# Kernel optimization log

Hardware: AMD Instinct MI355X
Metric: run time of the kernel (lower is better)

The kernel has to match this reference:

```python
import jax, jax.numpy as jnp
import numpy as np

B, S, E = 4, 1024, 1024
H, DK, HS = 16, 64, 64
FF = 4096
EPS = 1e-6


def _layernorm(x, g, b):
    mu = jnp.mean(x, axis=-1, keepdims=True)
    var = jnp.mean((x - mu) ** 2, axis=-1, keepdims=True)
    return (x - mu) * jax.lax.rsqrt(var + EPS) * g + b


def setup_inputs() -> dict:
    key = jax.random.key(0)
    ks = jax.random.split(key, 20)
    s_e = 1.0 / np.sqrt(E)
    s_ff = 1.0 / np.sqrt(FF)
    d = {
        "x": jax.random.normal(ks[0], (B, S, E), jnp.float32),
        "pos_encoding": jax.random.normal(ks[1], (S, S, 8), jnp.float32),
        # weights stored [in, out] (torch Linear transposed)
        "Wq": jax.random.normal(ks[2], (E, H * DK), jnp.float32) * s_e,
        "bq": jnp.zeros((H * DK,), jnp.float32),
        "Wk": jax.random.normal(ks[3], (E, H * DK), jnp.float32) * s_e,
        "bk": jnp.zeros((H * DK,), jnp.float32),
        "Wv": jax.random.normal(ks[4], (E, H * HS), jnp.float32) * s_e,
        "bv": jnp.zeros((H * HS,), jnp.float32),
        "Wo": jax.random.normal(ks[5], (H * HS, E), jnp.float32) * s_e,
        "bo": jnp.zeros((E,), jnp.float32),
        "Wg": jax.random.normal(ks[6], (E, E), jnp.float32) * s_e,
        "bg": jnp.zeros((E,), jnp.float32),
        "Wf1": jax.random.normal(ks[7], (E, FF), jnp.float32) * s_e,
        "bf1": jnp.zeros((FF,), jnp.float32),
        "Wfg": jax.random.normal(ks[8], (E, FF), jnp.float32) * s_e,
        "bfg": jnp.zeros((FF,), jnp.float32),
        "Wf2": jax.random.normal(ks[9], (FF, E), jnp.float32) * s_ff,
        "bf2": jnp.zeros((E,), jnp.float32),
        "ln1_g": jnp.ones((E,), jnp.float32),
        "ln1_b": jnp.zeros((E,), jnp.float32),
        "ln2_g": jnp.ones((E,), jnp.float32),
        "ln2_b": jnp.zeros((E,), jnp.float32),
    }
    return d


def reference(x, pos_encoding, Wq, bq, Wk, bk, Wv, bv, Wo, bo, Wg, bg,
              Wf1, bf1, Wfg, bfg, Wf2, bf2, ln1_g, ln1_b, ln2_g, ln2_b):
    b, s, _ = x.shape
    q = (x @ Wq + bq).reshape(b, s, H, DK)
    k = (x @ Wk + bk).reshape(b, s, H, DK)
    v = (x @ Wv + bv).reshape(b, s, H, HS)
    scale = jnp.sqrt(jnp.float32(DK))
    # [b, h, q, k]
    scores = jnp.einsum("bqhd,bkhd->bhqk", q, k) / scale
    pos_bias = jnp.mean(pos_encoding[:s, :s, :], axis=-1)  # [s, s]
    scores = scores + pos_bias[None, None, :, :]
    probs = jax.nn.softmax(scores, axis=-1)
    ctx = jnp.einsum("bhqk,bkhd->bqhd", probs, v).reshape(b, s, H * HS)
    attn_out = ctx @ Wo + bo
    attn_out = jax.nn.sigmoid(x @ Wg + bg) * attn_out
    x1 = _layernorm(x + attn_out, ln1_g, ln1_b)
    ff = (x1 @ Wf1 + bf1) * jax.nn.sigmoid(x1 @ Wfg + bfg)
    ff = ff @ Wf2 + bf2
    return _layernorm(x1 + ff, ln2_g, ln2_b)
```

## Files before the change

kernel.cpp:

```cpp
#include <hip/hip_runtime.h>

constexpr int NB = 4, NS = 1024, NE = 1024, NH = 16, NFF = 4096;
constexpr int NM = NB * NS;

typedef short s8v __attribute__((ext_vector_type(8)));
typedef short s4v __attribute__((ext_vector_type(4)));
typedef float f4  __attribute__((ext_vector_type(4)));

__device__ __forceinline__ float b2f(unsigned short u) {
    union { unsigned int i; float f; } v; v.i = ((unsigned int)u) << 16; return v.f;
}
__device__ __forceinline__ unsigned short f2b(float f) {
    union { float f; unsigned int i; } v; v.f = f;
    unsigned int r = v.i + 0x7FFFu + ((v.i >> 16) & 1u);
    return (unsigned short)(r >> 16);
}
__device__ __forceinline__ float sigf(float x) { return 1.f / (1.f + __expf(-x)); }

#define GL2LDS(g, l) __builtin_amdgcn_global_load_lds( \
    (const __attribute__((address_space(1))) void*)(g), \
    (__attribute__((address_space(3))) void*)(l), 16, 0, 0)

__global__ __launch_bounds__(256) void cvt_x_kernel(
    const float* __restrict__ X, unsigned short* __restrict__ O)
{
    size_t i = ((size_t)blockIdx.x * 256 + threadIdx.x) * 8;
    f4 v0 = *(const f4*)(X + i), v1 = *(const f4*)(X + i + 4);
    s8v o;
#pragma unroll
    for (int j = 0; j < 4; j++) { o[j] = (short)f2b(v0[j]); o[4 + j] = (short)f2b(v1[j]); }
    *(s8v*)(O + i) = o;
}

__global__ __launch_bounds__(256) void cvt_t_kernel(
    const float* s0, const float* s1, const float* s2, const float* s3, const float* s4,
    unsigned short* d0, unsigned short* d1, unsigned short* d2, unsigned short* d3,
    unsigned short* d4, int K, int N)
{
    const int z = blockIdx.z;
    const float* W = (z == 0) ? s0 : (z == 1) ? s1 : (z == 2) ? s2 : (z == 3) ? s3 : s4;
    unsigned short* WT = (z == 0) ? d0 : (z == 1) ? d1 : (z == 2) ? d2 : (z == 3) ? d3 : d4;
    __shared__ unsigned short L[64][72];
    const int k0 = blockIdx.y * 64, n0 = blockIdx.x * 64;
    const int t = threadIdx.x;
    const int r = t >> 4, c4 = (t & 15) * 4;
#pragma unroll
    for (int p = 0; p < 4; p++) {
        int k = r + p * 16;
        f4 v = *(const f4*)&W[(size_t)(k0 + k) * N + n0 + c4];
#pragma unroll
        for (int i = 0; i < 4; i++) L[c4 + i][k] = f2b(v[i]);
    }
    __syncthreads();
    const int n = t >> 2, kc = (t & 3) * 16;
    s8v o0, o1;
#pragma unroll
    for (int i = 0; i < 8; i++) { o0[i] = (short)L[n][kc + i]; o1[i] = (short)L[n][kc + 8 + i]; }
    unsigned short* dst = WT + (size_t)(n0 + n) * K + k0 + kc;
    *(s8v*)dst = o0; *(s8v*)(dst + 8) = o1;
}

__global__ __launch_bounds__(256) void posmean_kernel(
    const float* __restrict__ pe, float* __restrict__ bias)
{
    int idx = blockIdx.x * 256 + threadIdx.x;
    const float* p = pe + (size_t)idx * 8;
    f4 v0 = *(const f4*)p, v1 = *(const f4*)(p + 4);
    float s = 0.f;
#pragma unroll
    for (int i = 0; i < 4; i++) s += v0[i] + v1[i];
    bias[idx] = (s * 0.125f - 8.0f) * 1.44269504f;
}

#define EPI_QKVG     0
#define EPI_GATE_RES 2
#define EPI_RES      4
#define EPI_BIAS     5

template <int EPI, int TM>
__global__ __launch_bounds__(256) void gemm_bt(
    const unsigned short* __restrict__ A,
    const unsigned short* __restrict__ BT,
    const float* b0p, const float* b1p, const float* b2p, const float* b3p,
    const unsigned short* ex1,
    const unsigned short* ex2,
    unsigned short* C, int M, int N, int K)
{
    constexpr int AR = 32 * TM;
    __shared__ short As0[AR * 32], As1[AR * 32];
    __shared__ short Bs0[128 * 32], Bs1[128 * 32];

    const int tid  = threadIdx.x;
    const int m0   = blockIdx.y * AR;
    const int n0   = blockIdx.x * 128;
    const int lane = tid & 63;
    const int wave = tid >> 6;
    const int wm   = (wave >> 1) * (16 * TM), wn = (wave & 1) * 64;
    const int quad = lane >> 4, lo = lane & 15;
    const int lrow = lane >> 2;
    const int lcol = (((lane & 3) ^ ((lane >> 4) & 3))) * 8;
    const int rcol = ((quad ^ ((lo >> 2) & 3))) * 8;

    f4 acc[TM][4];
#pragma unroll
    for (int i = 0; i < TM; i++)
#pragma unroll
        for (int j = 0; j < 4; j++)
#pragma unroll
            for (int r = 0; r < 4; r++) acc[i][j][r] = 0.f;

    const unsigned short* ga = A  + (size_t)(m0 + wave * (AR / 4) + lrow) * K + lcol;
    const unsigned short* gb = BT + (size_t)(n0 + wave * 32 + lrow) * K + lcol;
    short* lA0  = &As0[(wave * (AR / 4)) * 32];
    short* lA1  = &As1[(wave * (AR / 4)) * 32];
    short* lB00 = &Bs0[(wave * 32) * 32];
    short* lB01 = &Bs0[(wave * 32 + 16) * 32];
    short* lB10 = &Bs1[(wave * 32) * 32];
    short* lB11 = &Bs1[(wave * 32 + 16) * 32];

    for (int k0 = 0; k0 < K; k0 += 64) {
#pragma unroll
        for (int t = 0; t < TM / 2; t++) {
            GL2LDS(ga + k0 +      (size_t)t * 16 * K, lA0 + t * 16 * 32);
            GL2LDS(ga + k0 + 32 + (size_t)t * 16 * K, lA1 + t * 16 * 32);
        }
        GL2LDS(gb + k0,               lB00);
        GL2LDS(gb + k0 + 16 * K,      lB01);
        GL2LDS(gb + k0 + 32,          lB10);
        GL2LDS(gb + k0 + 32 + 16 * K, lB11);
        __syncthreads();

        s8v af[TM], bf[4];
#pragma unroll
        for (int i = 0; i < TM; i++)
            af[i] = *(const s8v*)&As0[(wm + i * 16 + lo) * 32 + rcol];
#pragma unroll
        for (int j = 0; j < 4; j++)
            bf[j] = *(const s8v*)&Bs0[(wn + j * 16 + lo) * 32 + rcol];
#pragma unroll
        for (int i = 0; i < TM; i++)
#pragma unroll
            for (int j = 0; j < 4; j++)
                acc[i][j] = __builtin_amdgcn_mfma_f32_16x16x32_bf16(af[i], bf[j], acc[i][j], 0, 0, 0);
#pragma unroll
        for (int i = 0; i < TM; i++)
            af[i] = *(const s8v*)&As1[(wm + i * 16 + lo) * 32 + rcol];
#pragma unroll
        for (int j = 0; j < 4; j++)
            bf[j] = *(const s8v*)&Bs1[(wn + j * 16 + lo) * 32 + rcol];
#pragma unroll
        for (int i = 0; i < TM; i++)
#pragma unroll
            for (int j = 0; j < 4; j++)
                acc[i][j] = __builtin_amdgcn_mfma_f32_16x16x32_bf16(af[i], bf[j], acc[i][j], 0, 0, 0);
        __syncthreads();
    }

    const float* bp = b0p;
    bool do_sig = false;
    if (EPI == EPI_QKVG) {
        int seg = n0 >> 10;
        bp = (seg == 0) ? b0p : (seg == 1) ? b1p : (seg == 2) ? b2p : b3p;
        do_sig = (n0 >= 3072);
    }

#pragma unroll
    for (int i = 0; i < TM; i++) {
#pragma unroll
        for (int j = 0; j < 4; j++) {
#pragma unroll
            for (int r = 0; r < 4; r++) {
                int gm = m0 + wm + i * 16 + quad * 4 + r;
                int gn = n0 + wn + j * 16 + lo;
                size_t idx = (size_t)gm * N + gn;
                float v = acc[i][j][r] + (EPI == EPI_QKVG ? bp[gn & 1023] : bp[gn]);
                if (EPI == EPI_QKVG)          { if (do_sig) v = sigf(v); }
                else if (EPI == EPI_GATE_RES) v = b2f(ex1[idx]) + b2f(ex2[(size_t)gm * 4096 + gn]) * v;
                else if (EPI == EPI_RES)      v = b2f(ex1[idx]) + v;
                C[idx] = f2b(v);
            }
        }
    }
}

template <int TM>
__global__ __launch_bounds__(256) void gemm_ff(
    const unsigned short* __restrict__ A,
    const unsigned short* __restrict__ B1T,
    const unsigned short* __restrict__ B2T,
    const float* __restrict__ bias1, const float* __restrict__ bias2,
    unsigned short* __restrict__ C, int M, int N, int K)
{
    constexpr int AR = 32 * TM;
    __shared__ short As[AR * 32];
    __shared__ short B1s[128 * 32];
    __shared__ short B2s[128 * 32];

    const int tid  = threadIdx.x;
    const int m0   = blockIdx.y * AR;
    const int n0   = blockIdx.x * 128;
    const int lane = tid & 63;
    const int wave = tid >> 6;
    const int wm   = (wave >> 1) * (16 * TM), wn = (wave & 1) * 64;
    const int quad = lane >> 4, lo = lane & 15;
    const int lrow = lane >> 2;
    const int lcol = (((lane & 3) ^ ((lane >> 4) & 3))) * 8;
    const int rcol = ((quad ^ ((lo >> 2) & 3))) * 8;

    f4 accA[TM][4], accB[TM][4];
#pragma unroll
    for (int i = 0; i < TM; i++)
#pragma unroll
        for (int j = 0; j < 4; j++)
#pragma unroll
            for (int r = 0; r < 4; r++) { accA[i][j][r] = 0.f; accB[i][j][r] = 0.f; }

    const unsigned short* ga  = A   + (size_t)(m0 + wave * (AR / 4) + lrow) * K + lcol;
    const unsigned short* gb1 = B1T + (size_t)(n0 + wave * 32 + lrow) * K + lcol;
    const unsigned short* gb2 = B2T + (size_t)(n0 + wave * 32 + lrow) * K + lcol;
    short* lA   = &As[(wave * (AR / 4)) * 32];
    short* lB10 = &B1s[(wave * 32) * 32];
    short* lB11 = &B1s[(wave * 32 + 16) * 32];
    short* lB20 = &B2s[(wave * 32) * 32];
    short* lB21 = &B2s[(wave * 32 + 16) * 32];

    for (int k0 = 0; k0 < K; k0 += 32) {
#pragma unroll
        for (int t = 0; t < TM / 2; t++)
            GL2LDS(ga + k0 + (size_t)t * 16 * K, lA + t * 16 * 32);
        GL2LDS(gb1 + k0,          lB10);
        GL2LDS(gb1 + k0 + 16 * K, lB11);
        GL2LDS(gb2 + k0,          lB20);
        GL2LDS(gb2 + k0 + 16 * K, lB21);
        __syncthreads();

        s8v af[TM], b1f[4], b2f_[4];
#pragma unroll
        for (int i = 0; i < TM; i++)
            af[i] = *(const s8v*)&As[(wm + i * 16 + lo) * 32 + rcol];
#pragma unroll
        for (int j = 0; j < 4; j++) {
            b1f[j]  = *(const s8v*)&B1s[(wn + j * 16 + lo) * 32 + rcol];
            b2f_[j] = *(const s8v*)&B2s[(wn + j * 16 + lo) * 32 + rcol];
        }
#pragma unroll
        for (int i = 0; i < TM; i++)
#pragma unroll
            for (int j = 0; j < 4; j++) {
                accA[i][j] = __builtin_amdgcn_mfma_f32_16x16x32_bf16(af[i], b1f[j],  accA[i][j], 0, 0, 0);
                accB[i][j] = __builtin_amdgcn_mfma_f32_16x16x32_bf16(af[i], b2f_[j], accB[i][j], 0, 0, 0);
            }
        __syncthreads();
    }

#pragma unroll
    for (int i = 0; i < TM; i++) {
#pragma unroll
        for (int j = 0; j < 4; j++) {
#pragma unroll
            for (int r = 0; r < 4; r++) {
                int gm = m0 + wm + i * 16 + quad * 4 + r;
                int gn = n0 + wn + j * 16 + lo;
                float a = accA[i][j][r] + bias1[gn];
                float g = accB[i][j][r] + bias2[gn];
                C[(size_t)gm * N + gn] = f2b(a * sigf(g));
            }
        }
    }
}

__global__ __launch_bounds__(256) void attn_kernel(
    const unsigned short* __restrict__ QKVG, const float* __restrict__ bias,
    unsigned short* __restrict__ ctx)
{
    __shared__ short Ks[32 * 72];
    __shared__ short Vt[64 * 48];
    __shared__ short Ps[4][16 * 40];

    const int tid = threadIdx.x;
    const int lane = tid & 63, wave = tid >> 6;
    const int quad = lane >> 4, lo = lane & 15;
    const int bh = blockIdx.y;
    const int b = bh >> 4, h = bh & 15;
    const int q0 = blockIdx.x * 64 + wave * 16;
    const size_t base  = (size_t)b * NS * 4096 + (size_t)h * 64;
    const size_t baseK = base + 1024, baseV = base + 2048;
    constexpr float c1 = 0.125f * 1.44269504f;

    s8v aq0 = *(const s8v*)(QKVG + base + (size_t)(q0 + lo) * 4096 + quad * 8);
    s8v aq1 = *(const s8v*)(QKVG + base + (size_t)(q0 + lo) * 4096 + 32 + quad * 8);

    f4 accO[4];
    float l_r[4];
#pragma unroll
    for (int r = 0; r < 4; r++) {
        l_r[r] = 0.f;
#pragma unroll
        for (int j = 0; j < 4; j++) accO[j][r] = 0.f;
    }

    const int skv = tid >> 3, sd8 = (tid & 7) * 8;
    const int vkv = tid & 31, vd8 = (tid >> 5) * 8;
    const int pvk = 2 * (vkv & 15) + (vkv >> 4);

    s8v kk = *(const s8v*)(QKVG + baseK + (size_t)skv * 4096 + sd8);
    s8v vv = *(const s8v*)(QKVG + baseV + (size_t)vkv * 4096 + vd8);

    for (int kv0 = 0; kv0 < NS; kv0 += 32) {
        *(s8v*)&Ks[skv * 72 + sd8] = kk;
#pragma unroll
        for (int i = 0; i < 8; i++) Vt[(vd8 + i) * 48 + pvk] = (short)vv[i];
        __syncthreads();

        s8v kkn = kk, vvn = vv;
        if (kv0 + 32 < NS) {
            kkn = *(const s8v*)(QKVG + baseK + (size_t)(kv0 + 32 + skv) * 4096 + sd8);
            vvn = *(const s8v*)(QKVG + baseV + (size_t)(kv0 + 32 + vkv) * 4096 + vd8);
        }

        f4 sc[2];
#pragma unroll
        for (int cb = 0; cb < 2; cb++) {
            s8v bk0 = *(const s8v*)&Ks[(cb * 16 + lo) * 72 + quad * 8];
            s8v bk1 = *(const s8v*)&Ks[(cb * 16 + lo) * 72 + 32 + quad * 8];
            f4 z;
#pragma unroll
            for (int r = 0; r < 4; r++) z[r] = 0.f;
            z = __builtin_amdgcn_mfma_f32_16x16x32_bf16(aq0, bk0, z, 0, 0, 0);
            sc[cb] = __builtin_amdgcn_mfma_f32_16x16x32_bf16(aq1, bk1, z, 0, 0, 0);
        }

        int* PsI = (int*)&Ps[wave][0];
#pragma unroll
        for (int r = 0; r < 4; r++) {
            int qrow = q0 + quad * 4 + r;
            const float* bp = &bias[(size_t)qrow * NS + kv0];
            float p0 = exp2f(sc[0][r] * c1 + bp[lo]);
            float p1 = exp2f(sc[1][r] * c1 + bp[16 + lo]);
            l_r[r] += p0 + p1;
            unsigned int pk = (unsigned int)f2b(p0) | ((unsigned int)f2b(p1) << 16);
            PsI[(quad * 4 + r) * 20 + lo] = (int)pk;
        }
        s8v pf = *(const s8v*)&Ps[wave][lo * 40 + quad * 8];
#pragma unroll
        for (int j = 0; j < 4; j++) {
            s8v bv = *(const s8v*)&Vt[(j * 16 + lo) * 48 + quad * 8];
            accO[j] = __builtin_amdgcn_mfma_f32_16x16x32_bf16(pf, bv, accO[j], 0, 0, 0);
        }
        __syncthreads();
        kk = kkn; vv = vvn;
    }

#pragma unroll
    for (int r = 0; r < 4; r++) {
        float l = l_r[r];
#pragma unroll
        for (int d = 1; d < 16; d <<= 1) l += __shfl_xor(l, d, 64);
        l_r[r] = 1.f / l;
    }
#pragma unroll
    for (int j = 0; j < 4; j++)
#pragma unroll
        for (int r = 0; r < 4; r++) {
            int qrow = q0 + quad * 4 + r;
            ctx[((size_t)b * NS + qrow) * 1024 + h * 64 + j * 16 + lo] = f2b(accO[j][r] * l_r[r]);
        }
}

__global__ __launch_bounds__(256) void ln_kernel(
    const unsigned short* __restrict__ X, const float* __restrict__ g,
    const float* __restrict__ bb, void* __restrict__ out, int outF32)
{
    const int row = blockIdx.x;
    const unsigned short* xr = X + (size_t)row * NE;
    s4v xv = *(const s4v*)(xr + threadIdx.x * 4);
    float v[4], s = 0.f, ss = 0.f;
#pragma unroll
    for (int i = 0; i < 4; i++) {
        v[i] = b2f((unsigned short)xv[i]);
        s += v[i]; ss += v[i] * v[i];
    }
#pragma unroll
    for (int d = 1; d < 64; d <<= 1) { s += __shfl_xor(s, d, 64); ss += __shfl_xor(ss, d, 64); }
    __shared__ float red[8];
    int wave = threadIdx.x >> 6, lane = threadIdx.x & 63;
    if (lane == 0) { red[wave] = s; red[4 + wave] = ss; }
    __syncthreads();
    s  = red[0] + red[1] + red[2] + red[3];
    ss = red[4] + red[5] + red[6] + red[7];
    float mu = s * (1.f / NE);
    float var = ss * (1.f / NE) - mu * mu;
    float rstd = rsqrtf(fmaxf(var, 0.f) + 1e-6f);
#pragma unroll
    for (int i = 0; i < 4; i++) {
        int c = threadIdx.x * 4 + i;
        size_t idx = (size_t)row * NE + c;
        float o = (v[i] - mu) * rstd * g[c] + bb[c];
        if (outF32) ((float*)out)[idx] = o;
        else        ((unsigned short*)out)[idx] = f2b(o);
    }
}

extern "C" void kernel_launch(void* const* d_in, const int* in_sizes, int n_in,
                              void* d_out, int out_size, void* d_ws, size_t ws_size,
                              hipStream_t stream)
{
    const float* x    = (const float*)d_in[0];
    const float* pe   = (const float*)d_in[1];
    const float* Wq   = (const float*)d_in[2];
    const float* bq   = (const float*)d_in[3];
    const float* Wk   = (const float*)d_in[4];
    const float* bk   = (const float*)d_in[5];
    const float* Wv   = (const float*)d_in[6];
    const float* bv   = (const float*)d_in[7];
    const float* Wo   = (const float*)d_in[8];
    const float* bo   = (const float*)d_in[9];
    const float* Wg   = (const float*)d_in[10];
    const float* bg   = (const float*)d_in[11];
    const float* Wf1  = (const float*)d_in[12];
    const float* bf1  = (const float*)d_in[13];
    const float* Wfg  = (const float*)d_in[14];
    const float* bfg  = (const float*)d_in[15];
    const float* Wf2  = (const float*)d_in[16];
    const float* bf2  = (const float*)d_in[17];
    const float* ln1g = (const float*)d_in[18];
    const float* ln1b = (const float*)d_in[19];
    const float* ln2g = (const float*)d_in[20];
    const float* ln2b = (const float*)d_in[21];

    char* ws = (char*)d_ws;
    unsigned short* xb    = (unsigned short*)ws;
    unsigned short* WTq   = (unsigned short*)(ws + ( 8ull << 20));
    unsigned short* WoT   = (unsigned short*)(ws + (16ull << 20));
    unsigned short* Wf1T  = (unsigned short*)(ws + (18ull << 20));
    unsigned short* WfgT  = (unsigned short*)(ws + (26ull << 20));
    unsigned short* Wf2T  = (unsigned short*)(ws + (34ull << 20));
    float*          biasP = (float*)(ws + (42ull << 20));
    unsigned short* QKVG  = (unsigned short*)(ws + (46ull << 20));
    unsigned short* T1 = xb;
    unsigned short* Cx = WTq;
    unsigned short* X1 = WTq;
    unsigned short* H1 = QKVG;
    unsigned short* T2 = xb;

    dim3 blk(256);
    cvt_x_kernel<<<dim3(NM * NE / (256 * 8)), blk, 0, stream>>>(x, xb);
    cvt_t_kernel<<<dim3(16, 16, 5), blk, 0, stream>>>(
        Wq, Wk, Wv, Wg, Wo,
        WTq + 0ull * 1024 * 1024, WTq + 1ull * 1024 * 1024,
        WTq + 2ull * 1024 * 1024, WTq + 3ull * 1024 * 1024, WoT, NE, NE);
    cvt_t_kernel<<<dim3(64, 16, 2), blk, 0, stream>>>(
        Wf1, Wfg, nullptr, nullptr, nullptr,
        Wf1T, WfgT, nullptr, nullptr, nullptr, NE, NFF);
    cvt_t_kernel<<<dim3(16, 64, 1), blk, 0, stream>>>(
        Wf2, nullptr, nullptr, nullptr, nullptr,
        Wf2T, nullptr, nullptr, nullptr, nullptr, NFF, NE);
    posmean_kernel<<<dim3(NS * NS / 256), blk, 0, stream>>>(pe, biasP);

    gemm_bt<EPI_QKVG, 4><<<dim3(32, 32), blk, 0, stream>>>(
        xb, WTq, bq, bk, bv, bg, nullptr, nullptr, QKVG, NM, 4096, NE);

    attn_kernel<<<dim3(NS / 64, NB * NH), blk, 0, stream>>>(QKVG, biasP, Cx);

    gemm_bt<EPI_GATE_RES, 2><<<dim3(8, 64), blk, 0, stream>>>(
        Cx, WoT, bo, nullptr, nullptr, nullptr, xb, QKVG + 3072, T1, NM, NE, NE);
    ln_kernel<<<dim3(NM), blk, 0, stream>>>(T1, ln1g, ln1b, X1, 0);

    gemm_ff<2><<<dim3(32, 64), blk, 0, stream>>>(
        X1, Wf1T, WfgT, bf1, bfg, H1, NM, NFF, NE);

    gemm_bt<EPI_RES, 2><<<dim3(8, 64), blk, 0, stream>>>(
        H1, Wf2T, bf2, nullptr, nullptr, nullptr, X1, nullptr, T2, NM, NE, NFF);
    ln_kernel<<<dim3(NM), blk, 0, stream>>>(T2, ln2g, ln2b, d_out, 1);
}
```

Before: 510.9 us.

## Rewrite gated FFN GEMM as 8-wave 256x128 tile with multi-stage LDS pipeline

```diff
diff --git a/kernel.cpp b/kernel.cpp
--- a/kernel.cpp
+++ b/kernel.cpp
@@ -183,87 +183,138 @@
     }
 }
 
-template <int TM>
-__global__ __launch_bounds__(256) void gemm_ff(
+__global__ __launch_bounds__(512, 1) void gemm_ff8(
     const unsigned short* __restrict__ A,
     const unsigned short* __restrict__ B1T,
     const unsigned short* __restrict__ B2T,
     const float* __restrict__ bias1, const float* __restrict__ bias2,
-    unsigned short* __restrict__ C, int M, int N, int K)
-{
-    constexpr int AR = 32 * TM;
-    __shared__ short As[AR * 32];
-    __shared__ short B1s[128 * 32];
-    __shared__ short B2s[128 * 32];
+    unsigned short* __restrict__ C)
+{
+    __shared__ short Lds[8 * 8192];
 
     const int tid  = threadIdx.x;
-    const int m0   = blockIdx.y * AR;
-    const int n0   = blockIdx.x * 128;
-    const int lane = tid & 63;
-    const int wave = tid >> 6;
-    const int wm   = (wave >> 1) * (16 * TM), wn = (wave & 1) * 64;
-    const int quad = lane >> 4, lo = lane & 15;
-    const int lrow = lane >> 2;
-    const int lcol = (((lane & 3) ^ ((lane >> 4) & 3))) * 8;
-    const int rcol = ((quad ^ ((lo >> 2) & 3))) * 8;
-
-    f4 accA[TM][4], accB[TM][4];
-#pragma unroll
-    for (int i = 0; i < TM; i++)
+    const int ln   = tid & 63, wv = tid >> 6;
+    const int wr   = wv >> 1, wc = wv & 1;
+    const int quad = ln >> 4, lo = ln & 15;
+    const int m0   = blockIdx.y * 256, n0 = blockIdx.x * 128;
+
+    const int rowst = wv * 8 + (ln >> 3);
+    const int cosrc = ((ln & 7) ^ (ln >> 3)) * 8;
+    short* const ldst0 = &Lds[(wv * 8) * 64];
+
+    f4 accA[4][4], accB[4][4];
+#pragma unroll
+    for (int i = 0; i < 4; i++)
 #pragma unroll
         for (int j = 0; j < 4; j++)
 #pragma unroll
             for (int r = 0; r < 4; r++) { accA[i][j][r] = 0.f; accB[i][j][r] = 0.f; }
 
-    const unsigned short* ga  = A   + (size_t)(m0 + wave * (AR / 4) + lrow) * K + lcol;
-    const unsigned short* gb1 = B1T + (size_t)(n0 + wave * 32 + lrow) * K + lcol;
-    const unsigned short* gb2 = B2T + (size_t)(n0 + wave * 32 + lrow) * K + lcol;
-    short* lA   = &As[(wave * (AR / 4)) * 32];
-    short* lB10 = &B1s[(wave * 32) * 32];
-    short* lB11 = &B1s[(wave * 32 + 16) * 32];
-    short* lB20 = &B2s[(wave * 32) * 32];
-    short* lB21 = &B2s[(wave * 32 + 16) * 32];
-
-    for (int k0 = 0; k0 < K; k0 += 32) {
-#pragma unroll
-        for (int t = 0; t < TM / 2; t++)
-            GL2LDS(ga + k0 + (size_t)t * 16 * K, lA + t * 16 * 32);
-        GL2LDS(gb1 + k0,          lB10);
-        GL2LDS(gb1 + k0 + 16 * K, lB11);
-        GL2LDS(gb2 + k0,          lB20);
-        GL2LDS(gb2 + k0 + 16 * K, lB21);
-        __syncthreads();
-
-        s8v af[TM], b1f[4], b2f_[4];
-#pragma unroll
-        for (int i = 0; i < TM; i++)
-            af[i] = *(const s8v*)&As[(wm + i * 16 + lo) * 32 + rcol];
+    auto stage_half = [&](int h) {
+        if (h >= 64) return;
+        const int tt = h >> 2, kind = h & 3, slot = h & 7;
+        const unsigned short* gsrc;
+        if (kind == 0)      gsrc = A   + (size_t)(m0 + rowst) * 1024 + tt * 64 + cosrc;
+        else if (kind == 1) gsrc = A   + (size_t)(m0 + 128 + rowst) * 1024 + tt * 64 + cosrc;
+        else if (kind == 2) gsrc = B1T + (size_t)(n0 + rowst) * 1024 + tt * 64 + cosrc;
+        else                gsrc = B2T + (size_t)(n0 + rowst) * 1024 + tt * 64 + cosrc;
+        short* ldst = ldst0 + slot * 8192;
+        GL2LDS(gsrc,                     ldst);
+        GL2LDS(gsrc + (size_t)64 * 1024, ldst + 64 * 64);
+    };
+
+    int aoff[2], boff[2];
+#pragma unroll
+    for (int kh = 0; kh < 2; kh++) {
+        const int sw = (((kh * 4 + quad) ^ (lo & 7)) * 8);
+        aoff[kh] = (((wr & 1) * 64 + lo) * 64) + sw;
+        boff[kh] = ((wc * 64 + lo) * 64) + sw;
+    }
+    const int slA = wr >> 1;
+
+#pragma unroll
+    for (int h = 0; h < 5; h++) stage_half(h);
+    asm volatile("s_waitcnt vmcnt(2)" ::: "memory");
+    __builtin_amdgcn_s_barrier();
+
+    for (int t = 0; t < 16; t++) {
+        const int p4 = (t & 1) * 4;
+        const short* LA  = &Lds[(p4 + slA) * 8192];
+        const short* LB1 = &Lds[(p4 + 2) * 8192];
+        const short* LB2 = &Lds[(p4 + 3) * 8192];
+        const int hb = 4 * t;
+        s8v af[4], bf[4];
+
+#pragma unroll
+        for (int i = 0; i < 4; i++) af[i] = *(const s8v*)&LA[aoff[0] + i * 1024];
+#pragma unroll
+        for (int j = 0; j < 4; j++) bf[j] = *(const s8v*)&LB1[boff[0] + j * 1024];
+        stage_half(hb + 5);
+        __builtin_amdgcn_s_barrier();
+        __builtin_amdgcn_s_setprio(1);
+#pragma unroll
+        for (int i = 0; i < 4; i++)
+#pragma unroll
+            for (int j = 0; j < 4; j++)
+                accA[i][j] = __builtin_amdgcn_mfma_f32_16x16x32_bf16(af[i], bf[j], accA[i][j], 0, 0, 0);
+        __builtin_amdgcn_s_setprio(0);
+        __builtin_amdgcn_s_barrier();
+
+#pragma unroll
+        for (int j = 0; j < 4; j++) bf[j] = *(const s8v*)&LB2[boff[0] + j * 1024];
+        stage_half(hb + 6);
+        __builtin_amdgcn_s_barrier();
+        __builtin_amdgcn_s_setprio(1);
+#pragma unroll
+        for (int i = 0; i < 4; i++)
+#pragma unroll
+            for (int j = 0; j < 4; j++)
+                accB[i][j] = __builtin_amdgcn_mfma_f32_16x16x32_bf16(af[i], bf[j], accB[i][j], 0, 0, 0);
+        __builtin_amdgcn_s_setprio(0);
+        __builtin_amdgcn_s_barrier();
+
+#pragma unroll
+        for (int i = 0; i < 4; i++) af[i] = *(const s8v*)&LA[aoff[1] + i * 1024];
+#pragma unroll
+        for (int j = 0; j < 4; j++) bf[j] = *(const s8v*)&LB1[boff[1] + j * 1024];
+        stage_half(hb + 7);
+        __builtin_amdgcn_s_barrier();
+        __builtin_amdgcn_s_setprio(1);
+#pragma unroll
+        for (int i = 0; i < 4; i++)
+#pragma unroll
+            for (int j = 0; j < 4; j++)
+                accA[i][j] = __builtin_amdgcn_mfma_f32_16x16x32_bf16(af[i], bf[j], accA[i][j], 0, 0, 0);
+        __builtin_amdgcn_s_setprio(0);
+        __builtin_amdgcn_s_barrier();
+
+#pragma unroll
+        for (int j = 0; j < 4; j++) bf[j] = *(const s8v*)&LB2[boff[1] + j * 1024];
+        stage_half(hb + 8);
+        __builtin_amdgcn_s_barrier();
+        __builtin_amdgcn_s_setprio(1);
+#pragma unroll
+        for (int i = 0; i < 4; i++)
+#pragma unroll
+            for (int j = 0; j < 4; j++)
+                accB[i][j] = __builtin_amdgcn_mfma_f32_16x16x32_bf16(af[i], bf[j], accB[i][j], 0, 0, 0);
+        __builtin_amdgcn_s_setprio(0);
+        if (t < 14)       { asm volatile("s_waitcnt vmcnt(2)" ::: "memory"); }
+        else if (t == 14) { asm volatile("s_waitcnt vmcnt(0)" ::: "memory"); }
+        __builtin_amdgcn_s_barrier();
+    }
+
+#pragma unroll
+    for (int i = 0; i < 4; i++) {
 #pragma unroll
         for (int j = 0; j < 4; j++) {
-            b1f[j]  = *(const s8v*)&B1s[(wn + j * 16 + lo) * 32 + rcol];
-            b2f_[j] = *(const s8v*)&B2s[(wn + j * 16 + lo) * 32 + rcol];
-        }
-#pragma unroll
-        for (int i = 0; i < TM; i++)
-#pragma unroll
-            for (int j = 0; j < 4; j++) {
-                accA[i][j] = __builtin_amdgcn_mfma_f32_16x16x32_bf16(af[i], b1f[j],  accA[i][j], 0, 0, 0);
-                accB[i][j] = __builtin_amdgcn_mfma_f32_16x16x32_bf16(af[i], b2f_[j], accB[i][j], 0, 0, 0);
-            }
-        __syncthreads();
-    }
-
-#pragma unroll
-    for (int i = 0; i < TM; i++) {
-#pragma unroll
-        for (int j = 0; j < 4; j++) {
 #pragma unroll
             for (int r = 0; r < 4; r++) {
-                int gm = m0 + wm + i * 16 + quad * 4 + r;
-                int gn = n0 + wn + j * 16 + lo;
+                int gm = m0 + wr * 64 + i * 16 + quad * 4 + r;
+                int gn = n0 + wc * 64 + j * 16 + lo;
                 float a = accA[i][j][r] + bias1[gn];
                 float g = accB[i][j][r] + bias2[gn];
-                C[(size_t)gm * N + gn] = f2b(a * sigf(g));
+                C[(size_t)gm * 4096 + gn] = f2b(a * sigf(g));
             }
         }
     }
@@ -466,8 +517,8 @@
         Cx, WoT, bo, nullptr, nullptr, nullptr, xb, QKVG + 3072, T1, NM, NE, NE);
     ln_kernel<<<dim3(NM), blk, 0, stream>>>(T1, ln1g, ln1b, X1, 0);
 
-    gemm_ff<2><<<dim3(32, 64), blk, 0, stream>>>(
-        X1, Wf1T, WfgT, bf1, bfg, H1, NM, NFF, NE);
+    gemm_ff8<<<dim3(NFF / 128, NM / 256), dim3(512), 0, stream>>>(
+        X1, Wf1T, WfgT, bf1, bfg, H1);
 
     gemm_bt<EPI_RES, 2><<<dim3(8, 64), blk, 0, stream>>>(
         H1, Wf2T, bf2, nullptr, nullptr, nullptr, X1, nullptr, T2, NM, NE, NFF);
```

Measured after the change: 474.1 us. 7.2% less time.
